# Kernel tuning notes

Measured on AMD Instinct MI355X. Metric: run time of the kernel, lower is better.

## Reference

```python
import jax, jax.numpy as jnp
import numpy as np

N, E, B = 100000, 1600000, 512
NE, EE, H = 32, 32, 64
SCALE = float(2**48 - 1)


def _mlp2(x, W1, b1, W2, b2):
    # Linear -> ReLU -> Linear
    return jax.nn.relu(x @ W1 + b1) @ W2 + b2


def _gine(x, src, dst, e, W1, b1, W2, b2, n):
    # GINEConv (eps=0): nn(x + sum_j relu(x_j + e_ij))
    m = jax.nn.relu(x[src] + e)                      # [E, d] gather + edge add
    agg = jax.ops.segment_sum(m, dst, num_segments=n)  # scatter-add to targets
    return _mlp2(x + agg, W1, b1, W2, b2)


def _encode(names, edge_index, edge_attr, batch,
            idW1, idb1, idW2, idb2, edW1, edb1, edW2, edb2,
            c1W1, c1b1, c1W2, c1b2, c2W1, c2b1, c2W2, c2b2, linW, linb):
    norm = jnp.clip((names.astype(jnp.float32) + 2.0) / SCALE, 0.0, 1.0)[:, None]
    x = _mlp2(norm, idW1, idb1, idW2, idb2)          # [N, NE]
    e = _mlp2(edge_attr, edW1, edb1, edW2, edb2)     # [E, EE]
    src, dst = edge_index[0], edge_index[1]
    x = jax.nn.relu(_gine(x, src, dst, e, c1W1, c1b1, c1W2, c1b2, N))
    e2 = e @ linW + linb                             # edge lin for conv2 (EE->H)
    x = jax.nn.relu(_gine(x, src, dst, e2, c2W1, c2b1, c2W2, c2b2, N))
    sums = jax.ops.segment_sum(x, batch, num_segments=B)
    cnt = jax.ops.segment_sum(jnp.ones((x.shape[0],), x.dtype), batch, num_segments=B)
    return sums / jnp.maximum(cnt, 1.0)[:, None]     # global_mean_pool


def setup_inputs() -> dict:
    key = jax.random.key(0)
    ks = iter(jax.random.split(key, 64))
    def w(shape):
        return jax.random.normal(next(ks), shape, dtype=jnp.float32) * 0.05
    d = {}
    d['node_names_s'] = jax.random.randint(next(ks), (N,), 0, 1000000)
    d['edge_index_s'] = jax.random.randint(next(ks), (2, E), 0, N)
    d['edge_attr_s'] = jax.random.uniform(next(ks), (E, 1), dtype=jnp.float32)
    d['batch_s'] = jnp.sort(jax.random.randint(next(ks), (N,), 0, B))
    d['node_names_g'] = jax.random.randint(next(ks), (N,), 0, 1000000)
    d['edge_index_g'] = jax.random.randint(next(ks), (2, E), 0, N)
    d['edge_attr_g'] = jax.random.uniform(next(ks), (E, 1), dtype=jnp.float32)
    d['batch_g'] = jnp.sort(jax.random.randint(next(ks), (N,), 0, B))
    d['depth'] = jax.random.uniform(next(ks), (B,), dtype=jnp.float32)
    # shared encoders
    d['idW1'], d['idb1'], d['idW2'], d['idb2'] = w((1, NE)), w((NE,)), w((NE, NE)), w((NE,))
    d['edW1'], d['edb1'], d['edW2'], d['edb2'] = w((1, EE)), w((EE,)), w((EE, EE)), w((EE,))
    # state convs
    d['s1W1'], d['s1b1'], d['s1W2'], d['s1b2'] = w((NE, H)), w((H,)), w((H, H)), w((H,))
    d['s2W1'], d['s2b1'], d['s2W2'], d['s2b2'] = w((H, H)), w((H,)), w((H, H)), w((H,))
    d['s2linW'], d['s2linb'] = w((EE, H)), w((H,))
    # goal convs
    d['g1W1'], d['g1b1'], d['g1W2'], d['g1b2'] = w((NE, H)), w((H,)), w((H, H)), w((H,))
    d['g2W1'], d['g2b1'], d['g2W2'], d['g2b2'] = w((H, H)), w((H,)), w((H, H)), w((H,))
    d['g2linW'], d['g2linb'] = w((EE, H)), w((H,))
    d['rW1'], d['rb1'], d['rW2'], d['rb2'] = w((2 * H + 1, H)), w((H,)), w((H, 1)), w((1,))
    return d


def reference(node_names_s, edge_index_s, edge_attr_s, batch_s,
              node_names_g, edge_index_g, edge_attr_g, batch_g, depth,
              idW1, idb1, idW2, idb2, edW1, edb1, edW2, edb2,
              s1W1, s1b1, s1W2, s1b2, s2W1, s2b1, s2W2, s2b2, s2linW, s2linb,
              g1W1, g1b1, g1W2, g1b2, g2W1, g2b1, g2W2, g2b2, g2linW, g2linb,
              rW1, rb1, rW2, rb2):
    s = _encode(node_names_s, edge_index_s, edge_attr_s, batch_s,
                idW1, idb1, idW2, idb2, edW1, edb1, edW2, edb2,
                s1W1, s1b1, s1W2, s1b2, s2W1, s2b1, s2W2, s2b2, s2linW, s2linb)
    g = _encode(node_names_g, edge_index_g, edge_attr_g, batch_g,
                idW1, idb1, idW2, idb2, edW1, edb1, edW2, edb2,
                g1W1, g1b1, g1W2, g1b2, g2W1, g2b1, g2W2, g2b2, g2linW, g2linb)
    z = jnp.concatenate([s, g, depth[:, None]], axis=1)  # [B, 2H+1]
    return _mlp2(z, rW1, rb1, rW2, rb2)[:, 0]            # [B]
```

## Files before the change

kernel.cpp:

```cpp
#include <hip/hip_runtime.h>
#include <hip/hip_fp16.h>
#include <stdint.h>

namespace {

constexpr int NN   = 100000;
constexpr int TN   = 2 * NN;
constexpr int NEDG = 1600000;
constexpr int TE   = 2 * NEDG;
constexpr int NBAT = 512;
constexpr int NSEG = 33;

constexpr int NC     = 782;
constexpr int TILE   = 4096;
constexpr int ABLK   = (TE + TILE - 1) / TILE;
constexpr int ENTCAP = 5120;

constexpr int CONVBLK = 2048;

constexpr int S1H = 20;
constexpr int S2H = 36;

constexpr int TAB_BP = 0;
constexpr int TAB_D1 = 32;
constexpr int TAB_C1 = TAB_D1 + NSEG * 32;
constexpr int TAB_E2 = TAB_C1 + NSEG * 32;
constexpr int TAB_TOTAL = TAB_E2 + 4 * NSEG * 64;

__device__ __forceinline__ float relu_(float x) { return fmaxf(x, 0.0f); }

__device__ __forceinline__ float4 shfl_xor4(float4 v, int m) {
  return make_float4(__shfl_xor(v.x, m), __shfl_xor(v.y, m),
                     __shfl_xor(v.z, m), __shfl_xor(v.w, m));
}

__device__ __forceinline__ __half2 bch(int u) {
  return *reinterpret_cast<__half2*>(&u);
}
__device__ __forceinline__ int f2h2(float a, float b) {
  __half2 h = __floats2half2_rn(a, b);
  return *reinterpret_cast<int*>(&h);
}

__device__ __forceinline__ int2 ldnt2(const int2* p) {
  long long v = __builtin_nontemporal_load(reinterpret_cast<const long long*>(p));
  int2 r;
  r.x = (int)(v & 0xFFFFFFFFll);
  r.y = (int)(((unsigned long long)v) >> 32);
  return r;
}

__global__ void build_tables(const float* __restrict__ eW1, const float* __restrict__ eb1,
                             const float* __restrict__ eW2, const float* __restrict__ eb2,
                             const float* __restrict__ sLW, const float* __restrict__ sLb,
                             const float* __restrict__ gLW, const float* __restrict__ gLb,
                             float* __restrict__ tabs) {
  __shared__ float traw[32];
  __shared__ float ts[32];
  __shared__ float dt[NSEG * 32];
  __shared__ float ct[NSEG * 32];
  int tid = threadIdx.x;
  if (tid < 32) {
    float w = eW1[tid], b = eb1[tid];
    traw[tid] = (w != 0.0f) ? (-b / w) : 3.0e38f;
  }
  __syncthreads();
  if (tid < 32) {
    float v = traw[tid];
    int r = 0;
    for (int j = 0; j < 32; ++j) {
      float u = traw[j];
      r += (u < v) || (u == v && j < tid);
    }
    ts[r] = v;
  }
  __syncthreads();
  if (tid < 32) tabs[TAB_BP + tid] = ts[tid];
  for (int idx = tid; idx < NSEG * 32; idx += blockDim.x) {
    int s = idx >> 5, j = idx & 31;
    float a;
    if (s == 0)            a = ts[0] - 1.0f;
    else if (s == NSEG - 1) a = ts[31] + 1.0f;
    else                   a = 0.5f * ts[s - 1] + 0.5f * ts[s];
    float d = 0.0f, c = 0.0f;
    for (int i = 0; i < 32; ++i) {
      float w = eW1[i], b = eb1[i];
      if (fmaf(a, w, b) > 0.0f) {
        float w2 = eW2[i * 32 + j];
        d = fmaf(w, w2, d);
        c = fmaf(b, w2, c);
      }
    }
    c += eb2[j];
    dt[idx] = d; ct[idx] = c;
    tabs[TAB_D1 + idx] = d;
    tabs[TAB_C1 + idx] = c;
  }
  __syncthreads();
  for (int idx = tid; idx < NSEG * 64; idx += blockDim.x) {
    int s = idx >> 6, k = idx & 63;
    float ds = 0.f, cs = 0.f, dg = 0.f, cg = 0.f;
    for (int j = 0; j < 32; ++j) {
      float dv = dt[s * 32 + j], cv = ct[s * 32 + j];
      float ws = sLW[j * 64 + k], wg = gLW[j * 64 + k];
      ds = fmaf(dv, ws, ds); cs = fmaf(cv, ws, cs);
      dg = fmaf(dv, wg, dg); cg = fmaf(cv, wg, cg);
    }
    cs += sLb[k]; cg += gLb[k];
    tabs[TAB_E2 + idx]                 = ds;
    tabs[TAB_E2 + NSEG * 64 + idx]     = cs;
    tabs[TAB_E2 + 2 * NSEG * 64 + idx] = dg;
    tabs[TAB_E2 + 3 * NSEG * 64 + idx] = cg;
  }
}

__global__ __launch_bounds__(256) void fused_front(
    const int* __restrict__ names_s, const int* __restrict__ names_g,
    const float* __restrict__ idW1, const float* __restrict__ idb1,
    const float* __restrict__ idW2, const float* __restrict__ idb2,
    const int* __restrict__ src_s, const int* __restrict__ dst_s, const float* __restrict__ attr_s,
    const int* __restrict__ src_g, const int* __restrict__ dst_g, const float* __restrict__ attr_g,
    const int* __restrict__ bat_s, const int* __restrict__ bat_g,
    const float* __restrict__ tabs,
    __half* __restrict__ x0h,
    int* __restrict__ gcur, int2* __restrict__ part,
    int* __restrict__ start_s, int* __restrict__ start_g) {
  __shared__ int hist[NC];
  __shared__ int lofs[NC];
  __shared__ int lcur[NC];
  __shared__ int2 sorted[TILE];
  __shared__ int addr[TILE];
  __shared__ int scanbuf[256];
// ... 75 lines not shown
      float a0 = idb2[j0], a1 = idb2[j0 + 1], a2 = idb2[j0 + 2], a3 = idb2[j0 + 3];
#pragma unroll
      for (int i = 0; i < 32; ++i) {
        float hv = h[i];
        a0 = fmaf(hv, idW2[i * 32 + j0],     a0);
        a1 = fmaf(hv, idW2[i * 32 + j0 + 1], a1);
        a2 = fmaf(hv, idW2[i * 32 + j0 + 2], a2);
        a3 = fmaf(hv, idW2[i * 32 + j0 + 3], a3);
      }
      outh[j0 >> 2] = make_int2(f2h2(a0, a1), f2h2(a2, a3));
    }
  } else {
    int blk = blockIdx.x - ABLK - 782;
    int half = blk >= 391;
    const int* bat = half ? bat_g : bat_s;
    int* start = half ? start_g : start_s;
    int i = (blk - half * 391) * 256 + t;
    if (i >= NN) return;
    int cur = bat[i];
    int prev = (i == 0) ? -1 : bat[i - 1];
    for (int b = prev + 1; b <= cur; ++b) start[b] = i;
    if (i == NN - 1) {
      for (int b = cur + 1; b <= NBAT; ++b) start[b] = NN;
    }
  }
}

__global__ __launch_bounds__(256) void partition_to_csr(
    const int* __restrict__ gcur,
    const int2* __restrict__ part,
    int* __restrict__ rowptr, int2* __restrict__ colattr) {
  __shared__ int2 outE[ENTCAP];
  __shared__ int hist[256];
  __shared__ int cur[256];
  __shared__ int sc[256];
  int t = threadIdx.x, b = blockIdx.x;
  {
    int acc = 0;
    for (int i = t; i < b; i += 256) acc += min(gcur[i], ENTCAP);
    sc[t] = acc;
    __syncthreads();
    for (int st = 128; st > 0; st >>= 1) {
      if (t < st) sc[t] += sc[t + st];
      __syncthreads();
    }
  }
  int obase = sc[0];
  if (b == 0 && t == 0) rowptr[TN] = TE;
  __syncthreads();
  hist[t] = 0;
  __syncthreads();
  int cnt = min(gcur[b], ENTCAP);
  int ibase = b * ENTCAP;
  for (int i = t; i < cnt; i += 256)
    atomicAdd(&hist[(part[ibase + i].x >> 17) & 255], 1);
  __syncthreads();
  int v = hist[t];
  sc[t] = v;
  __syncthreads();
  for (int st = 1; st < 256; st <<= 1) {
    int u = (t >= st) ? sc[t - st] : 0;
    __syncthreads();
    sc[t] += u;
    __syncthreads();
  }
  int excl = sc[t] - v;
  int gnode = b * 256 + t;
  if (gnode < TN) rowptr[gnode] = obase + excl;
  cur[t] = excl;
  __syncthreads();
  for (int i = t; i < cnt; i += 256) {
    int2 e = part[ibase + i];
    int dl = (e.x >> 17) & 255;
    int srcn = e.x & 0x1FFFF;
    int seg = (e.x >> 25) & 63;
    int pos = atomicAdd(&cur[dl], 1);
    float af = __int_as_float(e.y);
    outE[pos] = make_int2(srcn | (seg << 20), f2h2(af, af));
  }
  __syncthreads();
  for (int i = t; i < cnt; i += 256) colattr[obase + i] = outE[i];
}

__global__ __launch_bounds__(256) void conv1_dual(
    const __half* __restrict__ x0h,
    const int* __restrict__ rowptr, const int2* __restrict__ colattr,
    const float* __restrict__ tabs, float* __restrict__ hb) {
  __shared__ __half2 dt2[NSEG * S1H];
  __shared__ __half2 ct2[NSEG * S1H];
  for (int i = threadIdx.x; i < NSEG * 16; i += 256) {
    int s = i >> 4, j = i & 15;
    dt2[s * S1H + j] = __floats2half2_rn(tabs[TAB_D1 + s * 32 + 2 * j],
                                         tabs[TAB_D1 + s * 32 + 2 * j + 1]);
    ct2[s * S1H + j] = __floats2half2_rn(tabs[TAB_C1 + s * 32 + 2 * j],
                                         tabs[TAB_C1 + s * 32 + 2 * j + 1]);
  }
  __syncthreads();
  int lane = threadIdx.x & 63;
  int sub = lane & 7;
  int f0  = (lane >> 3) * 4;
  int h0  = (lane >> 3) * 2;
  int wid = blockIdx.x * 4 + (threadIdx.x >> 6);
  int nb = rowptr[wid], ne = rowptr[wid + 1];
  for (int n = wid; n < TN; n += 4 * CONVBLK) {
    int beg = nb, end = ne;
    int n2 = n + 4 * CONVBLK;
    if (n2 < TN) { nb = rowptr[n2]; ne = rowptr[n2 + 1]; }
    const __half* xb = x0h + (n >= NN ? (size_t)NN * 32 : 0);
    int2 sv = make_int2(0, 0);
    if (sub == 0) sv = *(const int2*)(x0h + (size_t)n * 32 + f0);
    float4 acc = make_float4(0.f, 0.f, 0.f, 0.f);
    for (int k = beg + sub; k < end; k += 16) {
      int2 ca0 = ldnt2(&colattr[k]);
      int kb = k + 8;
      bool has1 = kb < end;
      int2 ca1 = has1 ? ldnt2(&colattr[kb]) : ca0;
      unsigned p0 = (unsigned)ca0.x, p1 = (unsigned)ca1.x;
      int s0 = (int)(p0 & 0xFFFFFu), g0 = (int)(p0 >> 20);
      int s1 = (int)(p1 & 0xFFFFFu), g1 = (int)(p1 >> 20);
      __half2 az0 = bch(ca0.y);
      __half2 az1 = bch(ca1.y);
      int2 xv0 = *(const int2*)(xb + (size_t)s0 * 32 + f0);
      int2 xv1 = *(const int2*)(xb + (size_t)s1 * 32 + f0);
      int2 dv0 = *(const int2*)&dt2[g0 * S1H + h0];
      int2 cv0 = *(const int2*)&ct2[g0 * S1H + h0];
      __half2 v;
      float2 f;
      v = __hadd2(bch(xv0.x), __hfma2(az0, bch(dv0.x), bch(cv0.x)));
      f = __half22float2(v); acc.x += relu_(f.x); acc.y += relu_(f.y);
      v = __hadd2(bch(xv0.y), __hfma2(az0, bch(dv0.y), bch(cv0.y)));
      f = __half22float2(v); acc.z += relu_(f.x); acc.w += relu_(f.y);
      if (has1) {
        int2 dv1 = *(const int2*)&dt2[g1 * S1H + h0];
        int2 cv1 = *(const int2*)&ct2[g1 * S1H + h0];
        v = __hadd2(bch(xv1.x), __hfma2(az1, bch(dv1.x), bch(cv1.x)));
        f = __half22float2(v); acc.x += relu_(f.x); acc.y += relu_(f.y);
        v = __hadd2(bch(xv1.y), __hfma2(az1, bch(dv1.y), bch(cv1.y)));
        f = __half22float2(v); acc.z += relu_(f.x); acc.w += relu_(f.y);
      }
    }
#pragma unroll
    for (int m = 1; m < 8; m <<= 1) {
      float4 o = shfl_xor4(acc, m);
      acc.x += o.x; acc.y += o.y; acc.z += o.z; acc.w += o.w;
    }
    if (sub == 0) {
      float2 t0 = __half22float2(bch(sv.x)), t1 = __half22float2(bch(sv.y));
      *(float4*)(hb + (size_t)n * 32 + f0) =
          make_float4(t0.x + acc.x, t0.y + acc.y, t1.x + acc.z, t1.y + acc.w);
    }
  }
}

__global__ __launch_bounds__(256) void conv2_dual(
    const __half* __restrict__ x1h,
    const int* __restrict__ rowptr, const int2* __restrict__ colattr,
    const float* __restrict__ tabs, float* __restrict__ hb) {
  __shared__ __half2 dt2[NSEG * S2H];
  __shared__ __half2 ct2[NSEG * S2H];
  int halfg = blockIdx.x >= (CONVBLK / 2);
  const float* d2 = tabs + TAB_E2 + (size_t)halfg * 2 * NSEG * 64;
  for (int i = threadIdx.x; i < NSEG * 32; i += 256) {
    int s = i >> 5, j = i & 31;
    dt2[s * S2H + j] = __floats2half2_rn(d2[s * 64 + 2 * j], d2[s * 64 + 2 * j + 1]);
    ct2[s * S2H + j] = __floats2half2_rn(d2[NSEG * 64 + s * 64 + 2 * j],
                                         d2[NSEG * 64 + s * 64 + 2 * j + 1]);
  }
  __syncthreads();
  const __half* xb = x1h + (size_t)halfg * NN * 64;
  int lane = threadIdx.x & 63;
  int sub = lane & 7;
  int f0  = (lane >> 3) * 8;
  int h0  = (lane >> 3) * 4;
  int wid = (blockIdx.x - halfg * (CONVBLK / 2)) * 4 + (threadIdx.x >> 6);
  int nlim = halfg * NN + NN;
  int n0 = halfg * NN + wid;
  int nb = rowptr[n0], ne = rowptr[n0 + 1];
  for (int n = n0; n < nlim; n += 2 * CONVBLK) {
    int beg = nb, end = ne;
    int n2 = n + 2 * CONVBLK;
    if (n2 < nlim) { nb = rowptr[n2]; ne = rowptr[n2 + 1]; }
    int4 sv0 = make_int4(0, 0, 0, 0);
    if (sub == 0) sv0 = *(const int4*)(x1h + (size_t)n * 64 + f0);
    float4 accA = make_float4(0.f, 0.f, 0.f, 0.f);
    float4 accB = make_float4(0.f, 0.f, 0.f, 0.f);
    for (int k = beg + sub; k < end; k += 16) {
      int2 ca0 = ldnt2(&colattr[k]);
      int kb = k + 8;
      bool has1 = kb < end;
      int2 ca1 = has1 ? ldnt2(&colattr[kb]) : ca0;
      unsigned p0 = (unsigned)ca0.x, p1 = (unsigned)ca1.x;
      int s0 = (int)(p0 & 0xFFFFFu), g0 = (int)(p0 >> 20);
      int s1 = (int)(p1 & 0xFFFFFu), g1 = (int)(p1 >> 20);
      __half2 az0 = bch(ca0.y);
      __half2 az1 = bch(ca1.y);
      int4 xv0 = *(const int4*)(xb + (size_t)s0 * 64 + f0);
      int4 xv1 = *(const int4*)(xb + (size_t)s1 * 64 + f0);
      int4 dv0 = *(const int4*)&dt2[g0 * S2H + h0];
      int4 cv0 = *(const int4*)&ct2[g0 * S2H + h0];
      __half2 v;
      float2 f;
      v = __hadd2(bch(xv0.x), __hfma2(az0, bch(dv0.x), bch(cv0.x)));
      f = __half22float2(v); accA.x += relu_(f.x); accA.y += relu_(f.y);
      v = __hadd2(bch(xv0.y), __hfma2(az0, bch(dv0.y), bch(cv0.y)));
      f = __half22float2(v); accA.z += relu_(f.x); accA.w += relu_(f.y);
      v = __hadd2(bch(xv0.z), __hfma2(az0, bch(dv0.z), bch(cv0.z)));
      f = __half22float2(v); accB.x += relu_(f.x); accB.y += relu_(f.y);
      v = __hadd2(bch(xv0.w), __hfma2(az0, bch(dv0.w), bch(cv0.w)));
      f = __half22float2(v); accB.z += relu_(f.x); accB.w += relu_(f.y);
      if (has1) {
        int4 dv1 = *(const int4*)&dt2[g1 * S2H + h0];
        int4 cv1 = *(const int4*)&ct2[g1 * S2H + h0];
        v = __hadd2(bch(xv1.x), __hfma2(az1, bch(dv1.x), bch(cv1.x)));
        f = __half22float2(v); accA.x += relu_(f.x); accA.y += relu_(f.y);
        v = __hadd2(bch(xv1.y), __hfma2(az1, bch(dv1.y), bch(cv1.y)));
        f = __half22float2(v); accA.z += relu_(f.x); accA.w += relu_(f.y);
        v = __hadd2(bch(xv1.z), __hfma2(az1, bch(dv1.z), bch(cv1.z)));
        f = __half22float2(v); accB.x += relu_(f.x); accB.y += relu_(f.y);
        v = __hadd2(bch(xv1.w), __hfma2(az1, bch(dv1.w), bch(cv1.w)));
        f = __half22float2(v); accB.z += relu_(f.x); accB.w += relu_(f.y);
      }
    }
#pragma unroll
    for (int m = 1; m < 8; m <<= 1) {
      float4 oA = shfl_xor4(accA, m);
      float4 oB = shfl_xor4(accB, m);
      accA.x += oA.x; accA.y += oA.y; accA.z += oA.z; accA.w += oA.w;
      accB.x += oB.x; accB.y += oB.y; accB.z += oB.z; accB.w += oB.w;
    }
    if (sub == 0) {
      float2 t0 = __half22float2(bch(sv0.x)), t1 = __half22float2(bch(sv0.y));
      float2 t2 = __half22float2(bch(sv0.z)), t3 = __half22float2(bch(sv0.w));
      float* op = hb + (size_t)n * 64 + f0;
      *(float4*)op       = make_float4(t0.x + accA.x, t0.y + accA.y, t1.x + accA.z, t1.y + accA.w);
      *(float4*)(op + 4) = make_float4(t2.x + accB.x, t2.y + accB.y, t3.x + accB.z, t3.y + accB.w);
    }
  }
}

__global__ __launch_bounds__(256) void mlp1_dual(
    const float* __restrict__ hin,
    const float* __restrict__ sW1, const float* __restrict__ sb1,
    const float* __restrict__ sW2, const float* __restrict__ sb2,
    const float* __restrict__ gW1, const float* __restrict__ gb1,
    const float* __restrict__ gW2, const float* __restrict__ gb2,
    __half* __restrict__ hout) {
  constexpr int IN = 32;
  __shared__ float hsT[IN][65];
  __shared__ float ysT[64][65];
  int base = blockIdx.x * 64;
  for (int idx = threadIdx.x; idx < 64 * IN; idx += 256) {
    int node = idx / IN, k = idx - node * IN;
    hsT[k][node] = hin[(size_t)(base + node) * IN + k];
  }
  __syncthreads();
  int nt = threadIdx.x >> 4, jx = threadIdx.x & 15;
  int n0 = nt * 4, f0 = jx * 4;
  bool isg = (base + n0) >= NN;
  const float* W1 = isg ? gW1 : sW1;
  const float* b1 = isg ? gb1 : sb1;
  const float* W2 = isg ? gW2 : sW2;
  const float* b2 = isg ? gb2 : sb2;
  float4 acc0, acc1, acc2, acc3;
  {
    const float4 b = *(const float4*)(b1 + f0);
    acc0 = b; acc1 = b; acc2 = b; acc3 = b;
  }
  for (int k = 0; k < IN; ++k) {
    const float4 h = *(const float4*)&hsT[k][n0];
    const float4 w = *(const float4*)(W1 + k * 64 + f0);
    acc0.x = fmaf(h.x, w.x, acc0.x); acc0.y = fmaf(h.x, w.y, acc0.y);
    acc0.z = fmaf(h.x, w.z, acc0.z); acc0.w = fmaf(h.x, w.w, acc0.w);
    acc1.x = fmaf(h.y, w.x, acc1.x); acc1.y = fmaf(h.y, w.y, acc1.y);
    acc1.z = fmaf(h.y, w.z, acc1.z); acc1.w = fmaf(h.y, w.w, acc1.w);
    acc2.x = fmaf(h.z, w.x, acc2.x); acc2.y = fmaf(h.z, w.y, acc2.y);
    acc2.z = fmaf(h.z, w.z, acc2.z); acc2.w = fmaf(h.z, w.w, acc2.w);
    acc3.x = fmaf(h.w, w.x, acc3.x); acc3.y = fmaf(h.w, w.y, acc3.y);
    acc3.z = fmaf(h.w, w.z, acc3.z); acc3.w = fmaf(h.w, w.w, acc3.w);
  }
  ysT[f0 + 0][n0 + 0] = relu_(acc0.x); ysT[f0 + 1][n0 + 0] = relu_(acc0.y);
  ysT[f0 + 2][n0 + 0] = relu_(acc0.z); ysT[f0 + 3][n0 + 0] = relu_(acc0.w);
  ysT[f0 + 0][n0 + 1] = relu_(acc1.x); ysT[f0 + 1][n0 + 1] = relu_(acc1.y);
  ysT[f0 + 2][n0 + 1] = relu_(acc1.z); ysT[f0 + 3][n0 + 1] = relu_(acc1.w);
  ysT[f0 + 0][n0 + 2] = relu_(acc2.x); ysT[f0 + 1][n0 + 2] = relu_(acc2.y);
  ysT[f0 + 2][n0 + 2] = relu_(acc2.z); ysT[f0 + 3][n0 + 2] = relu_(acc2.w);
  ysT[f0 + 0][n0 + 3] = relu_(acc3.x); ysT[f0 + 1][n0 + 3] = relu_(acc3.y);
  ysT[f0 + 2][n0 + 3] = relu_(acc3.z); ysT[f0 + 3][n0 + 3] = relu_(acc3.w);
  __syncthreads();
  {
    const float4 b = *(const float4*)(b2 + f0);
    acc0 = b; acc1 = b; acc2 = b; acc3 = b;
  }
  for (int k = 0; k < 64; ++k) {
    const float4 h = *(const float4*)&ysT[k][n0];
    const float4 w = *(const float4*)(W2 + k * 64 + f0);
    acc0.x = fmaf(h.x, w.x, acc0.x); acc0.y = fmaf(h.x, w.y, acc0.y);
    acc0.z = fmaf(h.x, w.z, acc0.z); acc0.w = fmaf(h.x, w.w, acc0.w);
    acc1.x = fmaf(h.y, w.x, acc1.x); acc1.y = fmaf(h.y, w.y, acc1.y);
    acc1.z = fmaf(h.y, w.z, acc1.z); acc1.w = fmaf(h.y, w.w, acc1.w);
    acc2.x = fmaf(h.z, w.x, acc2.x); acc2.y = fmaf(h.z, w.y, acc2.y);
    acc2.z = fmaf(h.z, w.z, acc2.z); acc2.w = fmaf(h.z, w.w, acc2.w);
    acc3.x = fmaf(h.w, w.x, acc3.x); acc3.y = fmaf(h.w, w.y, acc3.y);
    acc3.z = fmaf(h.w, w.z, acc3.z); acc3.w = fmaf(h.w, w.w, acc3.w);
  }
  float4 o;
  o = make_float4(relu_(acc0.x), relu_(acc0.y), relu_(acc0.z), relu_(acc0.w));
  *(int2*)(hout + (size_t)(base + n0 + 0) * 64 + f0) = make_int2(f2h2(o.x, o.y), f2h2(o.z, o.w));
  o = make_float4(relu_(acc1.x), relu_(acc1.y), relu_(acc1.z), relu_(acc1.w));
  *(int2*)(hout + (size_t)(base + n0 + 1) * 64 + f0) = make_int2(f2h2(o.x, o.y), f2h2(o.z, o.w));
  o = make_float4(relu_(acc2.x), relu_(acc2.y), relu_(acc2.z), relu_(acc2.w));
  *(int2*)(hout + (size_t)(base + n0 + 2) * 64 + f0) = make_int2(f2h2(o.x, o.y), f2h2(o.z, o.w));
  o = make_float4(relu_(acc3.x), relu_(acc3.y), relu_(acc3.z), relu_(acc3.w));
  *(int2*)(hout + (size_t)(base + n0 + 3) * 64 + f0) = make_int2(f2h2(o.x, o.y), f2h2(o.z, o.w));
}

__global__ __launch_bounds__(256) void mlp2_pool_dual(
    const float* __restrict__ hin,
    const float* __restrict__ sW1, const float* __restrict__ sb1,
    const float* __restrict__ sW2, const float* __restrict__ sb2,
    const float* __restrict__ gW1, const float* __restrict__ gb1,
    const float* __restrict__ gW2, const float* __restrict__ gb2,
    const int* __restrict__ bat_s, const int* __restrict__ bat_g,
    float* __restrict__ psum) {
  constexpr int IN = 64;
  __shared__ float hsT[IN][65];
  __shared__ float ysT[64][65];
  __shared__ int pid[64];
  int base = blockIdx.x * 64;
  for (int idx = threadIdx.x; idx < 64 * IN; idx += 256) {
    int node = idx / IN, k = idx - node * IN;
    hsT[k][node] = hin[(size_t)(base + node) * IN + k];
  }
  if (threadIdx.x < 64) {
    int gb = base + threadIdx.x;
    pid[threadIdx.x] = (gb < NN) ? bat_s[gb] : (NBAT + bat_g[gb - NN]);
  }
  __syncthreads();
  int nt = threadIdx.x >> 4, jx = threadIdx.x & 15;
  int n0 = nt * 4, f0 = jx * 4;
  bool isg = (base + n0) >= NN;
  const float* W1 = isg ? gW1 : sW1;
  const float* b1 = isg ? gb1 : sb1;
  const float* W2 = isg ? gW2 : sW2;
  const float* b2 = isg ? gb2 : sb2;
  float4 acc0, acc1, acc2, acc3;
  {
    const float4 b = *(const float4*)(b1 + f0);
    acc0 = b; acc1 = b; acc2 = b; acc3 = b;
  }
  for (int k = 0; k < IN; ++k) {
    const float4 h = *(const float4*)&hsT[k][n0];
    const float4 w = *(const float4*)(W1 + k * 64 + f0);
    acc0.x = fmaf(h.x, w.x, acc0.x); acc0.y = fmaf(h.x, w.y, acc0.y);
    acc0.z = fmaf(h.x, w.z, acc0.z); acc0.w = fmaf(h.x, w.w, acc0.w);
    acc1.x = fmaf(h.y, w.x, acc1.x); acc1.y = fmaf(h.y, w.y, acc1.y);
    acc1.z = fmaf(h.y, w.z, acc1.z); acc1.w = fmaf(h.y, w.w, acc1.w);
    acc2.x = fmaf(h.z, w.x, acc2.x); acc2.y = fmaf(h.z, w.y, acc2.y);
    acc2.z = fmaf(h.z, w.z, acc2.z); acc2.w = fmaf(h.z, w.w, acc2.w);
    acc3.x = fmaf(h.w, w.x, acc3.x); acc3.y = fmaf(h.w, w.y, acc3.y);
    acc3.z = fmaf(h.w, w.z, acc3.z); acc3.w = fmaf(h.w, w.w, acc3.w);
  }
  ysT[f0 + 0][n0 + 0] = relu_(acc0.x); ysT[f0 + 1][n0 + 0] = relu_(acc0.y);
  ysT[f0 + 2][n0 + 0] = relu_(acc0.z); ysT[f0 + 3][n0 + 0] = relu_(acc0.w);
  ysT[f0 + 0][n0 + 1] = relu_(acc1.x); ysT[f0 + 1][n0 + 1] = relu_(acc1.y);
  ysT[f0 + 2][n0 + 1] = relu_(acc1.z); ysT[f0 + 3][n0 + 1] = relu_(acc1.w);
  ysT[f0 + 0][n0 + 2] = relu_(acc2.x); ysT[f0 + 1][n0 + 2] = relu_(acc2.y);
  ysT[f0 + 2][n0 + 2] = relu_(acc2.z); ysT[f0 + 3][n0 + 2] = relu_(acc2.w);
  ysT[f0 + 0][n0 + 3] = relu_(acc3.x); ysT[f0 + 1][n0 + 3] = relu_(acc3.y);
  ysT[f0 + 2][n0 + 3] = relu_(acc3.z); ysT[f0 + 3][n0 + 3] = relu_(acc3.w);
  __syncthreads();
  {
    const float4 b = *(const float4*)(b2 + f0);
    acc0 = b; acc1 = b; acc2 = b; acc3 = b;
  }
  for (int k = 0; k < 64; ++k) {
    const float4 h = *(const float4*)&ysT[k][n0];
    const float4 w = *(const float4*)(W2 + k * 64 + f0);
    acc0.x = fmaf(h.x, w.x, acc0.x); acc0.y = fmaf(h.x, w.y, acc0.y);
    acc0.z = fmaf(h.x, w.z, acc0.z); acc0.w = fmaf(h.x, w.w, acc0.w);
    acc1.x = fmaf(h.y, w.x, acc1.x); acc1.y = fmaf(h.y, w.y, acc1.y);
    acc1.z = fmaf(h.y, w.z, acc1.z); acc1.w = fmaf(h.y, w.w, acc1.w);
    acc2.x = fmaf(h.z, w.x, acc2.x); acc2.y = fmaf(h.z, w.y, acc2.y);
    acc2.z = fmaf(h.z, w.z, acc2.z); acc2.w = fmaf(h.z, w.w, acc2.w);
    acc3.x = fmaf(h.w, w.x, acc3.x); acc3.y = fmaf(h.w, w.y, acc3.y);
    acc3.z = fmaf(h.w, w.z, acc3.z); acc3.w = fmaf(h.w, w.w, acc3.w);
  }
  __syncthreads();
  ysT[f0 + 0][n0 + 0] = relu_(acc0.x); ysT[f0 + 1][n0 + 0] = relu_(acc0.y);
  ysT[f0 + 2][n0 + 0] = relu_(acc0.z); ysT[f0 + 3][n0 + 0] = relu_(acc0.w);
  ysT[f0 + 0][n0 + 1] = relu_(acc1.x); ysT[f0 + 1][n0 + 1] = relu_(acc1.y);
  ysT[f0 + 2][n0 + 1] = relu_(acc1.z); ysT[f0 + 3][n0 + 1] = relu_(acc1.w);
  ysT[f0 + 0][n0 + 2] = relu_(acc2.x); ysT[f0 + 1][n0 + 2] = relu_(acc2.y);
  ysT[f0 + 2][n0 + 2] = relu_(acc2.z); ysT[f0 + 3][n0 + 2] = relu_(acc2.w);
  ysT[f0 + 0][n0 + 3] = relu_(acc3.x); ysT[f0 + 1][n0 + 3] = relu_(acc3.y);
  ysT[f0 + 2][n0 + 3] = relu_(acc3.z); ysT[f0 + 3][n0 + 3] = relu_(acc3.w);
  __syncthreads();
  int c = threadIdx.x >> 6, f = threadIdx.x & 63;
  int cur = pid[c * 16];
  float run = 0.0f;
  for (int i = 0; i < 16; ++i) {
    int nx = c * 16 + i;
    int p = pid[nx];
    if (p != cur) { atomicAdd(&psum[(size_t)cur * 64 + f], run); run = 0.0f; cur = p; }
    run += ysT[f][nx];
  }
  atomicAdd(&psum[(size_t)cur * 64 + f], run);
}

__global__ __launch_bounds__(256) void regressor16(
    const float* __restrict__ psum,
    const int* __restrict__ start_s, const int* __restrict__ start_g,
    const float* __restrict__ depth,
    const float* __restrict__ W1, const float* __restrict__ b1,
    const float* __restrict__ W2, const float* __restrict__ b2,
    float* __restrict__ out) {
  __shared__ float zs[16][132];
  __shared__ float ys[64][17];
  __shared__ float inv_s[16], inv_g[16];
  int base = blockIdx.x * 16;
  if (threadIdx.x < 16) {
    int b = base + threadIdx.x;
    inv_s[threadIdx.x] = 1.0f / fmaxf((float)(start_s[b + 1] - start_s[b]), 1.0f);
    inv_g[threadIdx.x] = 1.0f / fmaxf((float)(start_g[b + 1] - start_g[b]), 1.0f);
  }
  __syncthreads();
  for (int i = threadIdx.x; i < 16 * 64; i += 256) {
    int ln = i >> 6, k = i & 63;
    zs[ln][k]      = psum[(size_t)(base + ln) * 64 + k] * inv_s[ln];
    zs[ln][64 + k] = psum[(size_t)(NBAT + base + ln) * 64 + k] * inv_g[ln];
  }
  if (threadIdx.x < 16) zs[threadIdx.x][128] = depth[base + threadIdx.x];
  __syncthreads();
  int g = threadIdx.x >> 4;
  int j = threadIdx.x & 15;
  int f0 = j * 4;
  float a0, a1, a2, a3;
  {
    const float4 b = *(const float4*)(b1 + f0);
    a0 = b.x; a1 = b.y; a2 = b.z; a3 = b.w;
  }
  for (int k = 0; k < 129; ++k) {
    float zv = zs[g][k];
    const float4 w = *(const float4*)(W1 + k * 64 + f0);
    a0 = fmaf(zv, w.x, a0); a1 = fmaf(zv, w.y, a1);
    a2 = fmaf(zv, w.z, a2); a3 = fmaf(zv, w.w, a3);
  }
  ys[f0 + 0][g] = relu_(a0);
  ys[f0 + 1][g] = relu_(a1);
  ys[f0 + 2][g] = relu_(a2);
  ys[f0 + 3][g] = relu_(a3);
  __syncthreads();
  float s = ys[f0 + 0][g] * W2[f0 + 0] + ys[f0 + 1][g] * W2[f0 + 1] +
            ys[f0 + 2][g] * W2[f0 + 2] + ys[f0 + 3][g] * W2[f0 + 3];
#pragma unroll
  for (int m = 1; m < 16; m <<= 1) s += __shfl_xor(s, m);
  if (j == 0) out[base + g] = s + b2[0];
}

}

extern "C" void kernel_launch(void* const* d_in, const int* in_sizes, int n_in,
                              void* d_out, int out_size, void* d_ws, size_t ws_size,
                              hipStream_t stream) {
  const int*   names_s = (const int*)d_in[0];
  const int*   ei_s    = (const int*)d_in[1];
  const float* ea_s    = (const float*)d_in[2];
  const int*   bat_s   = (const int*)d_in[3];
  const int*   names_g = (const int*)d_in[4];
  const int*   ei_g    = (const int*)d_in[5];
  const float* ea_g    = (const float*)d_in[6];
  const int*   bat_g   = (const int*)d_in[7];
  const float* depth   = (const float*)d_in[8];
  const float* idW1 = (const float*)d_in[9],  *idb1 = (const float*)d_in[10];
  const float* idW2 = (const float*)d_in[11], *idb2 = (const float*)d_in[12];
  const float* edW1 = (const float*)d_in[13], *edb1 = (const float*)d_in[14];
  const float* edW2 = (const float*)d_in[15], *edb2 = (const float*)d_in[16];
  const float* s1W1 = (const float*)d_in[17], *s1b1 = (const float*)d_in[18];
  const float* s1W2 = (const float*)d_in[19], *s1b2 = (const float*)d_in[20];
  const float* s2W1 = (const float*)d_in[21], *s2b1 = (const float*)d_in[22];
  const float* s2W2 = (const float*)d_in[23], *s2b2 = (const float*)d_in[24];
  const float* s2LW = (const float*)d_in[25], *s2Lb = (const float*)d_in[26];
  const float* g1W1 = (const float*)d_in[27], *g1b1 = (const float*)d_in[28];
  const float* g1W2 = (const float*)d_in[29], *g1b2 = (const float*)d_in[30];
  const float* g2W1 = (const float*)d_in[31], *g2b1 = (const float*)d_in[32];
  const float* g2W2 = (const float*)d_in[33], *g2b2 = (const float*)d_in[34];
  const float* g2LW = (const float*)d_in[35], *g2Lb = (const float*)d_in[36];
  const float* rW1  = (const float*)d_in[37], *rb1  = (const float*)d_in[38];
  const float* rW2  = (const float*)d_in[39], *rb2  = (const float*)d_in[40];
  (void)in_sizes; (void)n_in; (void)out_size; (void)ws_size;

  char* ws = (char*)d_ws;
  size_t off = 0;
  auto alloc = [&](size_t bytes) -> char* {
    char* p = ws + off;
    off += (bytes + 255) & ~(size_t)255;
    return p;
  };
  float* tabs    = (float*)alloc((size_t)TAB_TOTAL * 4);
  char*  act   = alloc((size_t)TN * 64 * 4 + (size_t)TN * 32 * 4);
  float* h2buf = (float*)act;
  float* h1buf = (float*)(act + (size_t)TN * 64 * 4);
  int2*  part  = (int2*)act;
  __half* x0h  = (__half*)alloc((size_t)TN * 32 * 2);
  __half* x1h  = (__half*)alloc((size_t)TN * 64 * 2);
  int2*  colattr = (int2*) alloc((size_t)TE * 8);
  int*   gcur    = (int*)  alloc((size_t)NC * 4);
  int*   rowptr  = (int*)  alloc((size_t)(TN + 1) * 4);
  int*   start_s = (int*)  alloc((size_t)(NBAT + 1) * 4);
  int*   start_g = (int*)  alloc((size_t)(NBAT + 1) * 4);
  float* psum    = (float*)alloc((size_t)2 * NBAT * 64 * 4);

  build_tables<<<1, 256, 0, stream>>>(edW1, edb1, edW2, edb2, s2LW, s2Lb, g2LW, g2Lb, tabs);
  hipMemsetAsync(gcur, 0, (size_t)NC * 4, stream);
  hipMemsetAsync(psum, 0, (size_t)2 * NBAT * 64 * 4, stream);

  fused_front<<<ABLK + 782 + 782, 256, 0, stream>>>(
      names_s, names_g, idW1, idb1, idW2, idb2,
      ei_s, ei_s + NEDG, ea_s, ei_g, ei_g + NEDG, ea_g,
      bat_s, bat_g, tabs, x0h, gcur, part, start_s, start_g);
  partition_to_csr<<<NC, 256, 0, stream>>>(gcur, part, rowptr, colattr);

  conv1_dual<<<CONVBLK, 256, 0, stream>>>(x0h, rowptr, colattr, tabs, h1buf);
  mlp1_dual<<<TN / 64, 256, 0, stream>>>(h1buf,
                                         s1W1, s1b1, s1W2, s1b2,
                                         g1W1, g1b1, g1W2, g1b2, x1h);
  conv2_dual<<<CONVBLK, 256, 0, stream>>>(x1h, rowptr, colattr, tabs, h2buf);
  mlp2_pool_dual<<<TN / 64, 256, 0, stream>>>(h2buf,
                                              s2W1, s2b1, s2W2, s2b2,
                                              g2W1, g2b1, g2W2, g2b2,
                                              bat_s, bat_g, psum);
  regressor16<<<32, 256, 0, stream>>>(psum, start_s, start_g, depth,
                                      rW1, rb1, rW2, rb2, (float*)d_out);
}
```

Baseline: 578.5 us.

## Fuse per-node MLPs and pooling into the GINE aggregation kernels

Merges the conv1 aggregation with the first GINE MLP, and the conv2 aggregation with the second MLP and mean-pool accumulation. Each wave now evaluates its node's MLP from shared rows, so the fp32 intermediate buffers and two launches go away. The trade-offs are less weight reuse than the old block-tiled GEMM and one global atomic per node-feature for pooling instead of run-length reduced sums. It also swaps the nontemporal colattr loads for ordinary loads.

```diff
diff --git a/kernel.cpp b/kernel.cpp
--- a/kernel.cpp
+++ b/kernel.cpp
@@ -40,14 +40,6 @@
 __device__ __forceinline__ int f2h2(float a, float b) {
   __half2 h = __floats2half2_rn(a, b);
   return *reinterpret_cast<int*>(&h);
-}
-
-__device__ __forceinline__ int2 ldnt2(const int2* p) {
-  long long v = __builtin_nontemporal_load(reinterpret_cast<const long long*>(p));
-  int2 r;
-  r.x = (int)(v & 0xFFFFFFFFll);
-  r.y = (int)(((unsigned long long)v) >> 32);
-  return r;
 }
 
 __global__ void build_tables(const float* __restrict__ eW1, const float* __restrict__ eb1,
@@ -289,12 +281,19 @@
   for (int i = t; i < cnt; i += 256) colattr[obase + i] = outE[i];
 }
 
-__global__ __launch_bounds__(256) void conv1_dual(
+__global__ __launch_bounds__(256) void conv1_mlp(
     const __half* __restrict__ x0h,
     const int* __restrict__ rowptr, const int2* __restrict__ colattr,
-    const float* __restrict__ tabs, float* __restrict__ hb) {
+    const float* __restrict__ tabs,
+    const float* __restrict__ sW1, const float* __restrict__ sb1,
+    const float* __restrict__ sW2, const float* __restrict__ sb2,
+    const float* __restrict__ gW1, const float* __restrict__ gb1,
+    const float* __restrict__ gW2, const float* __restrict__ gb2,
+    __half* __restrict__ x1h) {
   __shared__ __half2 dt2[NSEG * S1H];
   __shared__ __half2 ct2[NSEG * S1H];
+  __shared__ float hrow[4][32];
+  __shared__ float yrow[4][64];
   for (int i = threadIdx.x; i < NSEG * 16; i += 256) {
     int s = i >> 4, j = i & 15;
     dt2[s * S1H + j] = __floats2half2_rn(tabs[TAB_D1 + s * 32 + 2 * j],
@@ -303,25 +302,32 @@
                                          tabs[TAB_C1 + s * 32 + 2 * j + 1]);
   }
   __syncthreads();
+  int halfg = blockIdx.x >= (CONVBLK / 2);
+  const float* W1 = halfg ? gW1 : sW1;
+  const float* b1 = halfg ? gb1 : sb1;
+  const float* W2 = halfg ? gW2 : sW2;
+  const float* b2 = halfg ? gb2 : sb2;
+  const __half* xb = x0h + (size_t)halfg * NN * 32;
   int lane = threadIdx.x & 63;
+  int wv   = threadIdx.x >> 6;
   int sub = lane & 7;
   int f0  = (lane >> 3) * 4;
   int h0  = (lane >> 3) * 2;
-  int wid = blockIdx.x * 4 + (threadIdx.x >> 6);
-  int nb = rowptr[wid], ne = rowptr[wid + 1];
-  for (int n = wid; n < TN; n += 4 * CONVBLK) {
+  int wid = (blockIdx.x - halfg * (CONVBLK / 2)) * 4 + wv;
+  int nlim = halfg * NN + NN;
+  int n0 = halfg * NN + wid;
+  int nb = rowptr[n0], ne = rowptr[n0 + 1];
+  for (int n = n0; n < nlim; n += 2 * CONVBLK) {
     int beg = nb, end = ne;
-    int n2 = n + 4 * CONVBLK;
-    if (n2 < TN) { nb = rowptr[n2]; ne = rowptr[n2 + 1]; }
-    const __half* xb = x0h + (n >= NN ? (size_t)NN * 32 : 0);
-    int2 sv = make_int2(0, 0);
-    if (sub == 0) sv = *(const int2*)(x0h + (size_t)n * 32 + f0);
+    int n2 = n + 2 * CONVBLK;
+    if (n2 < nlim) { nb = rowptr[n2]; ne = rowptr[n2 + 1]; }
+    int2 sv = *(const int2*)(x0h + (size_t)n * 32 + f0);
     float4 acc = make_float4(0.f, 0.f, 0.f, 0.f);
     for (int k = beg + sub; k < end; k += 16) {
-      int2 ca0 = ldnt2(&colattr[k]);
+      int2 ca0 = colattr[k];
       int kb = k + 8;
       bool has1 = kb < end;
-      int2 ca1 = has1 ? ldnt2(&colattr[kb]) : ca0;
+      int2 ca1 = has1 ? colattr[kb] : ca0;
       unsigned p0 = (unsigned)ca0.x, p1 = (unsigned)ca1.x;
       int s0 = (int)(p0 & 0xFFFFFu), g0 = (int)(p0 >> 20);
       int s1 = (int)(p1 & 0xFFFFFu), g1 = (int)(p1 >> 20);
@@ -351,20 +357,43 @@
       float4 o = shfl_xor4(acc, m);
       acc.x += o.x; acc.y += o.y; acc.z += o.z; acc.w += o.w;
     }
-    if (sub == 0) {
+    {
       float2 t0 = __half22float2(bch(sv.x)), t1 = __half22float2(bch(sv.y));
-      *(float4*)(hb + (size_t)n * 32 + f0) =
-          make_float4(t0.x + acc.x, t0.y + acc.y, t1.x + acc.z, t1.y + acc.w);
-    }
-  }
-}
-
-__global__ __launch_bounds__(256) void conv2_dual(
+      if (sub == 0) {
+        hrow[wv][f0 + 0] = t0.x + acc.x;
+        hrow[wv][f0 + 1] = t0.y + acc.y;
+        hrow[wv][f0 + 2] = t1.x + acc.z;
+        hrow[wv][f0 + 3] = t1.y + acc.w;
+      }
+    }
+    __builtin_amdgcn_wave_barrier();
+    float a = b1[lane];
+#pragma unroll 8
+    for (int k = 0; k < 32; ++k) a = fmaf(hrow[wv][k], W1[k * 64 + lane], a);
+    yrow[wv][lane] = relu_(a);
+    __builtin_amdgcn_wave_barrier();
+    float c = b2[lane];
+#pragma unroll 8
+    for (int k = 0; k < 64; ++k) c = fmaf(yrow[wv][k], W2[k * 64 + lane], c);
+    x1h[(size_t)n * 64 + lane] = __float2half_rn(relu_(c));
+    __builtin_amdgcn_wave_barrier();
+  }
+}
+
+__global__ __launch_bounds__(256) void conv2_mlp_pool(
     const __half* __restrict__ x1h,
     const int* __restrict__ rowptr, const int2* __restrict__ colattr,
-    const float* __restrict__ tabs, float* __restrict__ hb) {
+    const float* __restrict__ tabs,
+    const float* __restrict__ sW1, const float* __restrict__ sb1,
+    const float* __restrict__ sW2, const float* __restrict__ sb2,
+    const float* __restrict__ gW1, const float* __restrict__ gb1,
+    const float* __restrict__ gW2, const float* __restrict__ gb2,
+    const int* __restrict__ bat_s, const int* __restrict__ bat_g,
+    float* __restrict__ psum) {
   __shared__ __half2 dt2[NSEG * S2H];
   __shared__ __half2 ct2[NSEG * S2H];
+  __shared__ float hrow[4][64];
+  __shared__ float yrow[4][64];
   int halfg = blockIdx.x >= (CONVBLK / 2);
   const float* d2 = tabs + TAB_E2 + (size_t)halfg * 2 * NSEG * 64;
   for (int i = threadIdx.x; i < NSEG * 32; i += 256) {
@@ -374,12 +403,17 @@
                                          d2[NSEG * 64 + s * 64 + 2 * j + 1]);
   }
   __syncthreads();
+  const float* W1 = halfg ? gW1 : sW1;
+  const float* b1 = halfg ? gb1 : sb1;
+  const float* W2 = halfg ? gW2 : sW2;
+  const float* b2 = halfg ? gb2 : sb2;
   const __half* xb = x1h + (size_t)halfg * NN * 64;
   int lane = threadIdx.x & 63;
+  int wv   = threadIdx.x >> 6;
   int sub = lane & 7;
   int f0  = (lane >> 3) * 8;
   int h0  = (lane >> 3) * 4;
-  int wid = (blockIdx.x - halfg * (CONVBLK / 2)) * 4 + (threadIdx.x >> 6);
+  int wid = (blockIdx.x - halfg * (CONVBLK / 2)) * 4 + wv;
   int nlim = halfg * NN + NN;
   int n0 = halfg * NN + wid;
   int nb = rowptr[n0], ne = rowptr[n0 + 1];
@@ -387,15 +421,14 @@
     int beg = nb, end = ne;
     int n2 = n + 2 * CONVBLK;
     if (n2 < nlim) { nb = rowptr[n2]; ne = rowptr[n2 + 1]; }
-    int4 sv0 = make_int4(0, 0, 0, 0);
-    if (sub == 0) sv0 = *(const int4*)(x1h + (size_t)n * 64 + f0);
+    int4 sv0 = *(const int4*)(x1h + (size_t)n * 64 + f0);
     float4 accA = make_float4(0.f, 0.f, 0.f, 0.f);
     float4 accB = make_float4(0.f, 0.f, 0.f, 0.f);
     for (int k = beg + sub; k < end; k += 16) {
-      int2 ca0 = ldnt2(&colattr[k]);
+      int2 ca0 = colattr[k];
       int kb = k + 8;
       bool has1 = kb < end;
-      int2 ca1 = has1 ? ldnt2(&colattr[kb]) : ca0;
+      int2 ca1 = has1 ? colattr[kb] : ca0;
       unsigned p0 = (unsigned)ca0.x, p1 = (unsigned)ca1.x;
       int s0 = (int)(p0 & 0xFFFFFu), g0 = (int)(p0 >> 20);
       int s1 = (int)(p1 & 0xFFFFFu), g1 = (int)(p1 >> 20);
@@ -435,183 +468,35 @@
       accA.x += oA.x; accA.y += oA.y; accA.z += oA.z; accA.w += oA.w;
       accB.x += oB.x; accB.y += oB.y; accB.z += oB.z; accB.w += oB.w;
     }
-    if (sub == 0) {
+    {
       float2 t0 = __half22float2(bch(sv0.x)), t1 = __half22float2(bch(sv0.y));
       float2 t2 = __half22float2(bch(sv0.z)), t3 = __half22float2(bch(sv0.w));
-      float* op = hb + (size_t)n * 64 + f0;
-      *(float4*)op       = make_float4(t0.x + accA.x, t0.y + accA.y, t1.x + accA.z, t1.y + accA.w);
-      *(float4*)(op + 4) = make_float4(t2.x + accB.x, t2.y + accB.y, t3.x + accB.z, t3.y + accB.w);
-    }
-  }
-}
-
-__global__ __launch_bounds__(256) void mlp1_dual(
-    const float* __restrict__ hin,
-    const float* __restrict__ sW1, const float* __restrict__ sb1,
-    const float* __restrict__ sW2, const float* __restrict__ sb2,
-    const float* __restrict__ gW1, const float* __restrict__ gb1,
-    const float* __restrict__ gW2, const float* __restrict__ gb2,
-    __half* __restrict__ hout) {
-  constexpr int IN = 32;
-  __shared__ float hsT[IN][65];
-  __shared__ float ysT[64][65];
-  int base = blockIdx.x * 64;
-  for (int idx = threadIdx.x; idx < 64 * IN; idx += 256) {
-    int node = idx / IN, k = idx - node * IN;
-    hsT[k][node] = hin[(size_t)(base + node) * IN + k];
-  }
-  __syncthreads();
-  int nt = threadIdx.x >> 4, jx = threadIdx.x & 15;
-  int n0 = nt * 4, f0 = jx * 4;
-  bool isg = (base + n0) >= NN;
-  const float* W1 = isg ? gW1 : sW1;
-  const float* b1 = isg ? gb1 : sb1;
-  const float* W2 = isg ? gW2 : sW2;
-  const float* b2 = isg ? gb2 : sb2;
-  float4 acc0, acc1, acc2, acc3;
-  {
-    const float4 b = *(const float4*)(b1 + f0);
-    acc0 = b; acc1 = b; acc2 = b; acc3 = b;
-  }
-  for (int k = 0; k < IN; ++k) {
-    const float4 h = *(const float4*)&hsT[k][n0];
-    const float4 w = *(const float4*)(W1 + k * 64 + f0);
-    acc0.x = fmaf(h.x, w.x, acc0.x); acc0.y = fmaf(h.x, w.y, acc0.y);
-    acc0.z = fmaf(h.x, w.z, acc0.z); acc0.w = fmaf(h.x, w.w, acc0.w);
-    acc1.x = fmaf(h.y, w.x, acc1.x); acc1.y = fmaf(h.y, w.y, acc1.y);
-    acc1.z = fmaf(h.y, w.z, acc1.z); acc1.w = fmaf(h.y, w.w, acc1.w);
-    acc2.x = fmaf(h.z, w.x, acc2.x); acc2.y = fmaf(h.z, w.y, acc2.y);
-    acc2.z = fmaf(h.z, w.z, acc2.z); acc2.w = fmaf(h.z, w.w, acc2.w);
-    acc3.x = fmaf(h.w, w.x, acc3.x); acc3.y = fmaf(h.w, w.y, acc3.y);
-    acc3.z = fmaf(h.w, w.z, acc3.z); acc3.w = fmaf(h.w, w.w, acc3.w);
-  }
-  ysT[f0 + 0][n0 + 0] = relu_(acc0.x); ysT[f0 + 1][n0 + 0] = relu_(acc0.y);
-  ysT[f0 + 2][n0 + 0] = relu_(acc0.z); ysT[f0 + 3][n0 + 0] = relu_(acc0.w);
-  ysT[f0 + 0][n0 + 1] = relu_(acc1.x); ysT[f0 + 1][n0 + 1] = relu_(acc1.y);
-  ysT[f0 + 2][n0 + 1] = relu_(acc1.z); ysT[f0 + 3][n0 + 1] = relu_(acc1.w);
-  ysT[f0 + 0][n0 + 2] = relu_(acc2.x); ysT[f0 + 1][n0 + 2] = relu_(acc2.y);
-  ysT[f0 + 2][n0 + 2] = relu_(acc2.z); ysT[f0 + 3][n0 + 2] = relu_(acc2.w);
-  ysT[f0 + 0][n0 + 3] = relu_(acc3.x); ysT[f0 + 1][n0 + 3] = relu_(acc3.y);
-  ysT[f0 + 2][n0 + 3] = relu_(acc3.z); ysT[f0 + 3][n0 + 3] = relu_(acc3.w);
-  __syncthreads();
-  {
-    const float4 b = *(const float4*)(b2 + f0);
-    acc0 = b; acc1 = b; acc2 = b; acc3 = b;
-  }
-  for (int k = 0; k < 64; ++k) {
-    const float4 h = *(const float4*)&ysT[k][n0];
-    const float4 w = *(const float4*)(W2 + k * 64 + f0);
-    acc0.x = fmaf(h.x, w.x, acc0.x); acc0.y = fmaf(h.x, w.y, acc0.y);
-    acc0.z = fmaf(h.x, w.z, acc0.z); acc0.w = fmaf(h.x, w.w, acc0.w);
-    acc1.x = fmaf(h.y, w.x, acc1.x); acc1.y = fmaf(h.y, w.y, acc1.y);
-    acc1.z = fmaf(h.y, w.z, acc1.z); acc1.w = fmaf(h.y, w.w, acc1.w);
-    acc2.x = fmaf(h.z, w.x, acc2.x); acc2.y = fmaf(h.z, w.y, acc2.y);
-    acc2.z = fmaf(h.z, w.z, acc2.z); acc2.w = fmaf(h.z, w.w, acc2.w);
-    acc3.x = fmaf(h.w, w.x, acc3.x); acc3.y = fmaf(h.w, w.y, acc3.y);
-    acc3.z = fmaf(h.w, w.z, acc3.z); acc3.w = fmaf(h.w, w.w, acc3.w);
-  }
-  float4 o;
-  o = make_float4(relu_(acc0.x), relu_(acc0.y), relu_(acc0.z), relu_(acc0.w));
-  *(int2*)(hout + (size_t)(base + n0 + 0) * 64 + f0) = make_int2(f2h2(o.x, o.y), f2h2(o.z, o.w));
-  o = make_float4(relu_(acc1.x), relu_(acc1.y), relu_(acc1.z), relu_(acc1.w));
-  *(int2*)(hout + (size_t)(base + n0 + 1) * 64 + f0) = make_int2(f2h2(o.x, o.y), f2h2(o.z, o.w));
-  o = make_float4(relu_(acc2.x), relu_(acc2.y), relu_(acc2.z), relu_(acc2.w));
-  *(int2*)(hout + (size_t)(base + n0 + 2) * 64 + f0) = make_int2(f2h2(o.x, o.y), f2h2(o.z, o.w));
-  o = make_float4(relu_(acc3.x), relu_(acc3.y), relu_(acc3.z), relu_(acc3.w));
-  *(int2*)(hout + (size_t)(base + n0 + 3) * 64 + f0) = make_int2(f2h2(o.x, o.y), f2h2(o.z, o.w));
-}
-
-__global__ __launch_bounds__(256) void mlp2_pool_dual(
-    const float* __restrict__ hin,
-    const float* __restrict__ sW1, const float* __restrict__ sb1,
-    const float* __restrict__ sW2, const float* __restrict__ sb2,
-    const float* __restrict__ gW1, const float* __restrict__ gb1,
-    const float* __restrict__ gW2, const float* __restrict__ gb2,
-    const int* __restrict__ bat_s, const int* __restrict__ bat_g,
-    float* __restrict__ psum) {
-  constexpr int IN = 64;
-  __shared__ float hsT[IN][65];
-  __shared__ float ysT[64][65];
-  __shared__ int pid[64];
-  int base = blockIdx.x * 64;
-  for (int idx = threadIdx.x; idx < 64 * IN; idx += 256) {
-    int node = idx / IN, k = idx - node * IN;
-    hsT[k][node] = hin[(size_t)(base + node) * IN + k];
-  }
-  if (threadIdx.x < 64) {
-    int gb = base + threadIdx.x;
-    pid[threadIdx.x] = (gb < NN) ? bat_s[gb] : (NBAT + bat_g[gb - NN]);
-  }
-  __syncthreads();
-  int nt = threadIdx.x >> 4, jx = threadIdx.x & 15;
-  int n0 = nt * 4, f0 = jx * 4;
-  bool isg = (base + n0) >= NN;
-  const float* W1 = isg ? gW1 : sW1;
-  const float* b1 = isg ? gb1 : sb1;
-  const float* W2 = isg ? gW2 : sW2;
-  const float* b2 = isg ? gb2 : sb2;
-  float4 acc0, acc1, acc2, acc3;
-  {
-    const float4 b = *(const float4*)(b1 + f0);
-    acc0 = b; acc1 = b; acc2 = b; acc3 = b;
-  }
-  for (int k = 0; k < IN; ++k) {
-    const float4 h = *(const float4*)&hsT[k][n0];
-    const float4 w = *(const float4*)(W1 + k * 64 + f0);
-    acc0.x = fmaf(h.x, w.x, acc0.x); acc0.y = fmaf(h.x, w.y, acc0.y);
-    acc0.z = fmaf(h.x, w.z, acc0.z); acc0.w = fmaf(h.x, w.w, acc0.w);
-    acc1.x = fmaf(h.y, w.x, acc1.x); acc1.y = fmaf(h.y, w.y, acc1.y);
-    acc1.z = fmaf(h.y, w.z, acc1.z); acc1.w = fmaf(h.y, w.w, acc1.w);
-    acc2.x = fmaf(h.z, w.x, acc2.x); acc2.y = fmaf(h.z, w.y, acc2.y);
-    acc2.z = fmaf(h.z, w.z, acc2.z); acc2.w = fmaf(h.z, w.w, acc2.w);
-    acc3.x = fmaf(h.w, w.x, acc3.x); acc3.y = fmaf(h.w, w.y, acc3.y);
-    acc3.z = fmaf(h.w, w.z, acc3.z); acc3.w = fmaf(h.w, w.w, acc3.w);
-  }
-  ysT[f0 + 0][n0 + 0] = relu_(acc0.x); ysT[f0 + 1][n0 + 0] = relu_(acc0.y);
-  ysT[f0 + 2][n0 + 0] = relu_(acc0.z); ysT[f0 + 3][n0 + 0] = relu_(acc0.w);
-  ysT[f0 + 0][n0 + 1] = relu_(acc1.x); ysT[f0 + 1][n0 + 1] = relu_(acc1.y);
-  ysT[f0 + 2][n0 + 1] = relu_(acc1.z); ysT[f0 + 3][n0 + 1] = relu_(acc1.w);
-  ysT[f0 + 0][n0 + 2] = relu_(acc2.x); ysT[f0 + 1][n0 + 2] = relu_(acc2.y);
-  ysT[f0 + 2][n0 + 2] = relu_(acc2.z); ysT[f0 + 3][n0 + 2] = relu_(acc2.w);
-  ysT[f0 + 0][n0 + 3] = relu_(acc3.x); ysT[f0 + 1][n0 + 3] = relu_(acc3.y);
-  ysT[f0 + 2][n0 + 3] = relu_(acc3.z); ysT[f0 + 3][n0 + 3] = relu_(acc3.w);
-  __syncthreads();
-  {
-    const float4 b = *(const float4*)(b2 + f0);
-    acc0 = b; acc1 = b; acc2 = b; acc3 = b;
-  }
-  for (int k = 0; k < 64; ++k) {
-    const float4 h = *(const float4*)&ysT[k][n0];
-    const float4 w = *(const float4*)(W2 + k * 64 + f0);
-    acc0.x = fmaf(h.x, w.x, acc0.x); acc0.y = fmaf(h.x, w.y, acc0.y);
-    acc0.z = fmaf(h.x, w.z, acc0.z); acc0.w = fmaf(h.x, w.w, acc0.w);
-    acc1.x = fmaf(h.y, w.x, acc1.x); acc1.y = fmaf(h.y, w.y, acc1.y);
-    acc1.z = fmaf(h.y, w.z, acc1.z); acc1.w = fmaf(h.y, w.w, acc1.w);
-    acc2.x = fmaf(h.z, w.x, acc2.x); acc2.y = fmaf(h.z, w.y, acc2.y);
-    acc2.z = fmaf(h.z, w.z, acc2.z); acc2.w = fmaf(h.z, w.w, acc2.w);
-    acc3.x = fmaf(h.w, w.x, acc3.x); acc3.y = fmaf(h.w, w.y, acc3.y);
-    acc3.z = fmaf(h.w, w.z, acc3.z); acc3.w = fmaf(h.w, w.w, acc3.w);
-  }
-  __syncthreads();
-  ysT[f0 + 0][n0 + 0] = relu_(acc0.x); ysT[f0 + 1][n0 + 0] = relu_(acc0.y);
-  ysT[f0 + 2][n0 + 0] = relu_(acc0.z); ysT[f0 + 3][n0 + 0] = relu_(acc0.w);
-  ysT[f0 + 0][n0 + 1] = relu_(acc1.x); ysT[f0 + 1][n0 + 1] = relu_(acc1.y);
-  ysT[f0 + 2][n0 + 1] = relu_(acc1.z); ysT[f0 + 3][n0 + 1] = relu_(acc1.w);
-  ysT[f0 + 0][n0 + 2] = relu_(acc2.x); ysT[f0 + 1][n0 + 2] = relu_(acc2.y);
-  ysT[f0 + 2][n0 + 2] = relu_(acc2.z); ysT[f0 + 3][n0 + 2] = relu_(acc2.w);
-  ysT[f0 + 0][n0 + 3] = relu_(acc3.x); ysT[f0 + 1][n0 + 3] = relu_(acc3.y);
-  ysT[f0 + 2][n0 + 3] = relu_(acc3.z); ysT[f0 + 3][n0 + 3] = relu_(acc3.w);
-  __syncthreads();
-  int c = threadIdx.x >> 6, f = threadIdx.x & 63;
-  int cur = pid[c * 16];
-  float run = 0.0f;
-  for (int i = 0; i < 16; ++i) {
-    int nx = c * 16 + i;
-    int p = pid[nx];
-    if (p != cur) { atomicAdd(&psum[(size_t)cur * 64 + f], run); run = 0.0f; cur = p; }
-    run += ysT[f][nx];
-  }
-  atomicAdd(&psum[(size_t)cur * 64 + f], run);
+      if (sub == 0) {
+        hrow[wv][f0 + 0] = t0.x + accA.x;
+        hrow[wv][f0 + 1] = t0.y + accA.y;
+        hrow[wv][f0 + 2] = t1.x + accA.z;
+        hrow[wv][f0 + 3] = t1.y + accA.w;
+        hrow[wv][f0 + 4] = t2.x + accB.x;
+        hrow[wv][f0 + 5] = t2.y + accB.y;
+        hrow[wv][f0 + 6] = t3.x + accB.z;
+        hrow[wv][f0 + 7] = t3.y + accB.w;
+      }
+    }
+    __builtin_amdgcn_wave_barrier();
+    float a = b1[lane];
+#pragma unroll 8
+    for (int k = 0; k < 64; ++k) a = fmaf(hrow[wv][k], W1[k * 64 + lane], a);
+    yrow[wv][lane] = relu_(a);
+    __builtin_amdgcn_wave_barrier();
+    float c = b2[lane];
+#pragma unroll 8
+    for (int k = 0; k < 64; ++k) c = fmaf(yrow[wv][k], W2[k * 64 + lane], c);
+    float y2 = relu_(c);
+    int nl = n - halfg * NN;
+    int pid = halfg ? (bat_g[nl] + NBAT) : bat_s[nl];
+    atomicAdd(&psum[(size_t)pid * 64 + lane], y2);
+    __builtin_amdgcn_wave_barrier();
+  }
 }
 
 __global__ __launch_bounds__(256) void regressor16(
@@ -704,10 +589,7 @@
     return p;
   };
   float* tabs    = (float*)alloc((size_t)TAB_TOTAL * 4);
-  char*  act   = alloc((size_t)TN * 64 * 4 + (size_t)TN * 32 * 4);
-  float* h2buf = (float*)act;
-  float* h1buf = (float*)(act + (size_t)TN * 64 * 4);
-  int2*  part  = (int2*)act;
+  int2*  part  = (int2*)alloc((size_t)NC * ENTCAP * 8);
   __half* x0h  = (__half*)alloc((size_t)TN * 32 * 2);
   __half* x1h  = (__half*)alloc((size_t)TN * 64 * 2);
   int2*  colattr = (int2*) alloc((size_t)TE * 8);
@@ -727,12 +609,10 @@
       bat_s, bat_g, tabs, x0h, gcur, part, start_s, start_g);
   partition_to_csr<<<NC, 256, 0, stream>>>(gcur, part, rowptr, colattr);
 
-  conv1_dual<<<CONVBLK, 256, 0, stream>>>(x0h, rowptr, colattr, tabs, h1buf);
-  mlp1_dual<<<TN / 64, 256, 0, stream>>>(h1buf,
+  conv1_mlp<<<CONVBLK, 256, 0, stream>>>(x0h, rowptr, colattr, tabs,
                                          s1W1, s1b1, s1W2, s1b2,
                                          g1W1, g1b1, g1W2, g1b2, x1h);
-  conv2_dual<<<CONVBLK, 256, 0, stream>>>(x1h, rowptr, colattr, tabs, h2buf);
-  mlp2_pool_dual<<<TN / 64, 256, 0, stream>>>(h2buf,
+  conv2_mlp_pool<<<CONVBLK, 256, 0, stream>>>(x1h, rowptr, colattr, tabs,
                                               s2W1, s2b1, s2W2, s2b2,
                                               g2W1, g2b1, g2W2, g2b2,
                                               bat_s, bat_g, psum);
```

Result: slower. 804.1 us (+39.0%).
